# Performance work log

Hardware: AMD Instinct MI355X
Metric: run time of the kernel (lower is better)

The kernel has to match this reference:

```python
import jax, jax.numpy as jnp
import numpy as np

C = 256
SCALE = 2
K = 3
GROUPS = 4


def _conv(x, w, b=None, groups=1, pad=0):
    y = jax.lax.conv_general_dilated(
        x, w, window_strides=(1, 1), padding=[(pad, pad), (pad, pad)],
        dimension_numbers=("NCHW", "OIHW", "NCHW"), feature_group_count=groups)
    if b is not None:
        y = y + b[None, :, None, None]
    return y


def _bn(x, g, b, m, v):
    # eval-mode BatchNorm2d, eps=1e-5
    scale = g / jnp.sqrt(v + 1e-5)
    return (x - m[None, :, None, None]) * scale[None, :, None, None] + b[None, :, None, None]


def _silu(x):
    return x * jax.nn.sigmoid(x)


def setup_inputs() -> dict:
    key = jax.random.key(0)
    ks = jax.random.split(key, 16)
    c = C
    s2k2 = SCALE ** 2 * K ** 2
    p = lambda k, shape, sc=0.05: jax.random.normal(k, shape, dtype=jnp.float32) * sc
    return {
        "x": jax.random.normal(ks[0], (8, c, 64, 64), dtype=jnp.float32),
        # kernel_compressor: 1x1, c -> c//2
        "Wkc": p(ks[1], (c // 2, c, 1, 1)), "bkc": p(ks[2], (c // 2,)),
        # kernel_predictor: 3x3 c//2 -> c//4, BN, SiLU, 1x1 -> s^2*k^2
        "Wkp1": p(ks[3], (c // 4, c // 2, 3, 3)), "bkp1": p(ks[4], (c // 4,)),
        "g1": 1.0 + p(ks[5], (c // 4,)), "be1": p(ks[6], (c // 4,)),
        "m1": p(ks[7], (c // 4,)), "v1": 1.0 + jax.random.uniform(ks[8], (c // 4,), dtype=jnp.float32),
        "Wkp2": p(ks[9], (s2k2, c // 4, 1, 1)), "bkp2": p(ks[10], (s2k2,)),
        # grouped 3x3 "deform" conv: c -> c, groups=4, no bias
        "Wdef": p(ks[11], (c, c // GROUPS, 3, 3)),
        # semantic gate
        "Wg1": p(ks[12], (c // 4, c, 1, 1)), "bg1": p(ks[13], (c // 4,)),
        "Wg2": p(ks[14], (c, c // 4, 1, 1)), "bg2": p(ks[15], (c,)),
    }


def reference(x, Wkc, bkc, Wkp1, bkp1, g1, be1, m1, v1, Wkp2, bkp2, Wdef, Wg1, bg1, Wg2, bg2):
    b, c, h, w = x.shape
    s, k = SCALE, K
    # --- dynamic reassembly kernel prediction ---
    comp = _conv(x, Wkc, bkc)                                    # (b, c/2, h, w)
    t = _silu(_bn(_conv(comp, Wkp1, bkp1, pad=1), g1, be1, m1, v1))
    kw = _conv(t, Wkp2, bkp2)                                    # (b, s^2*k^2, h, w)
    kw = kw.transpose(0, 2, 3, 1).reshape(b, h, w, s * s, k * k)
    kw = jax.nn.softmax(kw, axis=-1)
    # --- unfold (k x k patches, pad k//2), F.unfold ordering: kernel pos i*k+j ---
    xp = jnp.pad(x, ((0, 0), (0, 0), (1, 1), (1, 1)))
    patches = jnp.stack([xp[:, :, i:i + h, j:j + w]
                         for i in range(k) for j in range(k)], axis=-1)  # (b,c,h,w,k^2)
    kernel_out = jnp.einsum('bchwk,bhwsk->bhwsc', patches, kw)           # (b,h,w,s^2,c)
    kernel_out = kernel_out.transpose(0, 4, 1, 3, 2).reshape(b, c, h * s, w * s)
    # --- grouped conv branch + bilinear upsample (align_corners=False) ---
    enh = _conv(x, Wdef, None, groups=GROUPS, pad=1)
    up = jax.image.resize(enh, (b, c, h * s, w * s), method='linear')
    fused = kernel_out + up
    # --- SE-style semantic gate ---
    pooled = jnp.mean(fused, axis=(2, 3), keepdims=True)
    gate = jax.nn.sigmoid(_conv(_silu(_conv(pooled, Wg1, bg1)), Wg2, bg2))
    return fused * gate
```

## Files before the change

kernel.cpp:

```cpp
#include <hip/hip_runtime.h>
#include <hip/hip_bf16.h>

typedef __hip_bfloat16 bf16;
typedef __attribute__((ext_vector_type(8))) short short8;
typedef __attribute__((ext_vector_type(4))) float floatx4;

__device__ __forceinline__ float cvt(float v){ return v; }
__device__ __forceinline__ float cvt(bf16 v){ return __bfloat162float(v); }
__device__ __forceinline__ unsigned short f2bu(float f){
    union { float f; unsigned u; } uf; uf.f = f;
    unsigned u = uf.u;
    return (unsigned short)((u + 0x7FFFu + ((u>>16)&1u)) >> 16);
}
__device__ __forceinline__ float bu2f(unsigned short b){
    union { unsigned u; float f; } uf; uf.u = ((unsigned)b)<<16; return uf.f;
}
__device__ __forceinline__ floatx4 mfma16(short8 a, short8 b, floatx4 c){
    return __builtin_amdgcn_mfma_f32_16x16x32_bf16(a, b, c, 0, 0, 0);
}

constexpr size_t O_KW    = 0;
constexpr size_t O_ENH   = O_KW    + 1179648;
constexpr size_t O_XBT   = O_ENH   + 8388608;
constexpr size_t O_COMPB = O_XBT   + 4194304;
constexpr size_t O_TB    = O_COMPB + 2097152;
constexpr size_t O_POOL  = O_TB    + 1048576;
constexpr size_t O_GATE  = O_POOL  + 2048;
constexpr size_t O_WKC   = O_GATE  + 2048;
constexpr size_t O_BKC   = O_WKC   + 32768;
constexpr size_t O_WKP1  = O_BKC   + 128;
constexpr size_t O_ALPHA = O_WKP1  + 73728;
constexpr size_t O_BETA  = O_ALPHA + 64;
constexpr size_t O_WKP2  = O_BETA  + 64;
constexpr size_t O_BKP2  = O_WKP2  + 2304;
constexpr size_t O_WDEF  = O_BKP2  + 64;
constexpr size_t O_WG1   = O_WDEF  + 147456;
constexpr size_t O_BG1   = O_WG1   + 16384;
constexpr size_t O_WG2   = O_BG1   + 64;
constexpr size_t O_BG2   = O_WG2   + 16384;
constexpr size_t O_FLAG  = O_BG2   + 256;
constexpr size_t O_WKCB  = (O_FLAG + 1 + 3) & ~(size_t)3;
constexpr size_t O_WKP1B = O_WKCB  + 16384;
constexpr size_t O_WDEFB = O_WKP1B + 36864;

__global__ __launch_bounds__(256) void kdet(const unsigned* __restrict__ w, float* flag)
{
    int hits = 0;
    for (int i = threadIdx.x; i < 16384; i += 256){
        unsigned v = w[i];
        hits += (((v >> 7) & 0xFFu) == 0xFFu) ? 1 : 0;
    }
    __shared__ int sh[256];
    sh[threadIdx.x] = hits;
    __syncthreads();
    for (int o = 128; o > 0; o >>= 1){
        if (threadIdx.x < o) sh[threadIdx.x] += sh[threadIdx.x + o];
        __syncthreads();
    }
    if (threadIdx.x == 0) flag[0] = (sh[0] > 0) ? 1.0f : 0.0f;
}

template<typename T>
__device__ __forceinline__ void k0_body(
    const T* Wkc, const T* bkc, const T* Wkp1, const T* bkp1,
    const T* g1, const T* be1, const T* m1, const T* v1,
    const T* Wkp2, const T* bkp2, const T* Wdef,
    const T* Wg1, const T* bg1, const T* Wg2, const T* bg2,
    float* ws)
{
    int i = blockIdx.x*256 + threadIdx.x;
    if (i < 32768){ ws[O_WKC+i] = cvt(Wkc[i]); return; }  i -= 32768;
    if (i < 128)  { ws[O_BKC+i] = cvt(bkc[i]); return; }  i -= 128;
    if (i < 73728){ ws[O_WKP1+i]= cvt(Wkp1[i]); return; } i -= 73728;
    if (i < 64){
        float a = cvt(g1[i]) / sqrtf(cvt(v1[i]) + 1e-5f);
        ws[O_ALPHA+i] = a;
        ws[O_BETA+i]  = (cvt(bkp1[i]) - cvt(m1[i]))*a + cvt(be1[i]);
        return;
    } i -= 64;
    if (i < 2304) { ws[O_WKP2+i] = cvt(Wkp2[i]); return; } i -= 2304;
    if (i < 36)   { ws[O_BKP2+i] = cvt(bkp2[i]); return; } i -= 36;
    if (i < 147456){ ws[O_WDEF+i]= cvt(Wdef[i]); return; } i -= 147456;
    if (i < 16384){ ws[O_WG1+i]  = cvt(Wg1[i]); return; }  i -= 16384;
    if (i < 64)   { ws[O_BG1+i]  = cvt(bg1[i]); return; }  i -= 64;
    if (i < 16384){ ws[O_WG2+i]  = cvt(Wg2[i]); return; }  i -= 16384;
    if (i < 256)  { ws[O_BG2+i]  = cvt(bg2[i]); return; }  i -= 256;
    if (i < 2048) { ws[O_POOL+i] = 0.f; return; }
}

__global__ __launch_bounds__(256) void k0_prep(
    const void* Wkc, const void* bkc, const void* Wkp1, const void* bkp1,
    const void* g1, const void* be1, const void* m1, const void* v1,
    const void* Wkp2, const void* bkp2, const void* Wdef,
    const void* Wg1, const void* bg1, const void* Wg2, const void* bg2,
    float* ws)
{
    if (ws[O_FLAG] > 0.5f)
        k0_body<float>((const float*)Wkc,(const float*)bkc,(const float*)Wkp1,(const float*)bkp1,
                       (const float*)g1,(const float*)be1,(const float*)m1,(const float*)v1,
                       (const float*)Wkp2,(const float*)bkp2,(const float*)Wdef,
                       (const float*)Wg1,(const float*)bg1,(const float*)Wg2,(const float*)bg2, ws);
    else
        k0_body<bf16>((const bf16*)Wkc,(const bf16*)bkc,(const bf16*)Wkp1,(const bf16*)bkp1,
                      (const bf16*)g1,(const bf16*)be1,(const bf16*)m1,(const bf16*)v1,
                      (const bf16*)Wkp2,(const bf16*)bkp2,(const bf16*)Wdef,
                      (const bf16*)Wg1,(const bf16*)bg1,(const bf16*)Wg2,(const bf16*)bg2, ws);
}

__global__ __launch_bounds__(256) void k0b_pack(float* ws)
{
    unsigned short* wkcb  = (unsigned short*)(ws + O_WKCB);
    unsigned short* wkp1b = (unsigned short*)(ws + O_WKP1B);
    unsigned short* wdefb = (unsigned short*)(ws + O_WDEFB);
    int i = blockIdx.x*256 + threadIdx.x;
    if (i < 32768){
        int kc = i>>12, cout = (i>>5)&127, cil = i&31;
        wkcb[i] = f2bu(ws[O_WKC + (size_t)cout*256 + kc*32 + cil]);
        return;
    } i -= 32768;
    if (i < 73728){
        int ch = i/18432, r = i - ch*18432;
        int kp = r>>11, cout = (r>>5)&63, cil = r&31;
        wkp1b[i] = f2bu(ws[O_WKP1 + ((size_t)cout*128 + ch*32 + cil)*9 + kp]);
        return;
    } i -= 73728;
    if (i < 147456){
        int g = i/36864, r1 = i - g*36864;
        int ch = r1/18432, r2 = r1 - ch*18432;
        int kp = r2>>11, cout = (r2>>5)&63, cil = r2&31;
        wdefb[i] = f2bu(ws[O_WDEF + (((size_t)(g*64+cout))*64 + ch*32 + cil)*9 + kp]);
    }
}

template<typename T>
__device__ __forceinline__ void xcvt_body(const T* __restrict__ x, unsigned short* __restrict__ xbt)
{
    __shared__ float lT[64*65];
    const int b = blockIdx.y;
    const int ci0 = (blockIdx.x & 3) * 64;
    const int pos0 = (blockIdx.x >> 2) * 64;
    const int lane = threadIdx.x & 63;
    const int wrow = threadIdx.x >> 6;
    for (int i = wrow; i < 64; i += 4)
        lT[i*65 + lane] = cvt(x[((size_t)(b*256 + ci0 + i))*4096 + pos0 + lane]);
    __syncthreads();
    for (int u = threadIdx.x; u < 2048; u += 256){
        const int pr = u >> 5, pc = u & 31;
        unsigned lo = f2bu(lT[(2*pc)*65 + pr]);
        unsigned hi = f2bu(lT[(2*pc+1)*65 + pr]);
        *(unsigned*)&xbt[((size_t)(b*4096) + pos0 + pr)*256 + ci0 + 2*pc] = lo | (hi<<16);
    }
}

__global__ __launch_bounds__(256) void xcvt(const void* x, unsigned short* xbt, const float* flag)
{
    if (*flag > 0.5f) xcvt_body<float>((const float*)x, xbt);
    else              xcvt_body<bf16>((const bf16*)x, xbt);
}

__global__ __launch_bounds__(256) void k1_mfma(
    const unsigned short* __restrict__ xbt, const unsigned short* __restrict__ wb,
    const float* __restrict__ bias, unsigned short* __restrict__ compb)
{
    __shared__ __align__(16) short lA[128*32];
    __shared__ __align__(16) short lB[128*32];
    const int b = blockIdx.y, pos0 = blockIdx.x*128;
    const int tid = threadIdx.x;
    const int wave = tid>>6, lane = tid&63, q = lane>>4, r16 = lane&15;
    const int mh = (wave&1)*64, nh = (wave>>1)*64;
    floatx4 zero = {0.f,0.f,0.f,0.f};
    floatx4 acc[4][4];
    #pragma unroll
    for (int m=0;m<4;m++){ acc[m][0]=zero; acc[m][1]=zero; acc[m][2]=zero; acc[m][3]=zero; }

    for (int kc=0;kc<8;kc++){
        __syncthreads();
        {
            const short8* s = (const short8*)(wb + kc*4096);
            short8* d = (short8*)lA;
            d[tid] = s[tid]; d[tid+256] = s[tid+256];
        }
        {
            #pragma unroll
            for (int k=0;k<2;k++){
                const int u = tid + k*256;
                const int p = u>>2, part = u&3;
                *(short8*)&lB[p*32 + part*8] =
                    *(const short8*)(xbt + ((size_t)(b*4096)+pos0+p)*256 + kc*32 + part*8);
            }
        }
        __syncthreads();
        short8 af[4], bfr[4];
        #pragma unroll
        for (int mt=0;mt<4;mt++) af[mt]  = *(const short8*)&lA[(mh + mt*16 + r16)*32 + q*8];
        #pragma unroll
        for (int nt=0;nt<4;nt++) bfr[nt] = *(const short8*)&lB[(nh + nt*16 + r16)*32 + q*8];
        #pragma unroll
        for (int mt=0;mt<4;mt++)
            #pragma unroll
            for (int nt=0;nt<4;nt++)
                acc[mt][nt] = mfma16(af[mt], bfr[nt], acc[mt][nt]);
    }
    #pragma unroll
    for (int mt=0;mt<4;mt++){
        const int cb = mh + mt*16 + q*4;
        const float b0=bias[cb], b1=bias[cb+1], b2=bias[cb+2], b3=bias[cb+3];
        #pragma unroll
        for (int nt=0;nt<4;nt++){
            const int pos = pos0 + nh + nt*16 + r16;
            floatx4 v = acc[mt][nt];
            uint2 pk;
            pk.x = (unsigned)f2bu(v.x+b0) | ((unsigned)f2bu(v.y+b1)<<16);
            pk.y = (unsigned)f2bu(v.z+b2) | ((unsigned)f2bu(v.w+b3)<<16);
            *(uint2*)(compb + ((size_t)(b*4096)+pos)*128 + cb) = pk;
        }
    }
}

__global__ __launch_bounds__(256) void conv3x3_all(
    const unsigned short* __restrict__ xbt, const unsigned short* __restrict__ compb,
    const unsigned short* __restrict__ wkp1b, const unsigned short* __restrict__ wdefb,
    const float* __restrict__ alpha, const float* __restrict__ beta,
    unsigned short* __restrict__ tb, float* __restrict__ enh)
{
    __shared__ __align__(16) short lX[6*66*32];
    __shared__ __align__(16) short lW[9*64*32];
    const int row0 = blockIdx.x*4, b = blockIdx.y, z = blockIdx.z;
    const bool isKP = (z == 0);
    const int g = isKP ? 0 : (z-1);
    const int CICH  = isKP ? 4 : 2;
    const int CITOT = isKP ? 128 : 256;
    const int cibase = g*64;
    const unsigned short* src  = isKP ? compb : xbt;
    const unsigned short* wsrc = isKP ? wkp1b : (wdefb + (size_t)g*36864);
    const int tid = threadIdx.x;
    const int wave = tid>>6, lane = tid&63, q = lane>>4, r16 = lane&15;
    floatx4 zero = {0.f,0.f,0.f,0.f};
    floatx4 acc[4][4];
    #pragma unroll
    for (int m=0;m<4;m++){ acc[m][0]=zero; acc[m][1]=zero; acc[m][2]=zero; acc[m][3]=zero; }

    {
        short8 zz = {0,0,0,0,0,0,0,0};
        short8* d = (short8*)lX;
        for (int i = tid; i < 1584; i += 256) d[i] = zz;
    }

    for (int ch = 0; ch < CICH; ch++){
        __syncthreads();
        {
            const short8* s = (const short8*)(wsrc + ch*18432);
            short8* d = (short8*)lW;
            #pragma unroll
            for (int i=0;i<9;i++) d[tid + i*256] = s[tid + i*256];
        }
        {
            const int gc = tid>>2, part = tid&3;
            #pragma unroll
            for (int r=0;r<6;r++){
                const int gr = row0 - 1 + r;
                if ((unsigned)gr < 64u){
                    const unsigned short* sp = src +
                        ((size_t)(b*4096) + gr*64 + gc)*CITOT + cibase + ch*32 + part*8;
                    *(short8*)&lX[(r*66 + 1 + gc)*32 + part*8] = *(const short8*)sp;
                }
            }
        }
        __syncthreads();
        #pragma unroll
        for (int kp=0; kp<9; kp++){
            const int dr = kp/3, dc = kp - dr*3;
            short8 af[4], bfr[4];
            #pragma unroll
            for (int mt=0;mt<4;mt++)
                af[mt] = *(const short8*)&lW[(kp*64 + mt*16 + r16)*32 + q*8];
            #pragma unroll
            for (int nt=0;nt<4;nt++)
                bfr[nt] = *(const short8*)&lX[((wave+dr)*66 + nt*16 + r16 + dc)*32 + q*8];
            #pragma unroll
            for (int mt=0;mt<4;mt++)
                #pragma unroll
                for (int nt=0;nt<4;nt++)
                    acc[mt][nt] = mfma16(af[mt], bfr[nt], acc[mt][nt]);
        }
    }
    const int orow = row0 + wave;
    if (isKP){
        #pragma unroll
        for (int mt=0;mt<4;mt++){
            const int cb = mt*16 + q*4;
            const float a0=alpha[cb],a1=alpha[cb+1],a2=alpha[cb+2],a3=alpha[cb+3];
            const float e0=beta[cb],e1=beta[cb+1],e2=beta[cb+2],e3=beta[cb+3];
            #pragma unroll
            for (int nt=0;nt<4;nt++){
                const int pos = orow*64 + nt*16 + r16;
                floatx4 v = acc[mt][nt];
                float z0=v.x*a0+e0, z1=v.y*a1+e1, z2=v.z*a2+e2, z3=v.w*a3+e3;
                z0 = z0/(1.f+expf(-z0)); z1 = z1/(1.f+expf(-z1));
                z2 = z2/(1.f+expf(-z2)); z3 = z3/(1.f+expf(-z3));
                uint2 pk;
                pk.x = (unsigned)f2bu(z0) | ((unsigned)f2bu(z1)<<16);
                pk.y = (unsigned)f2bu(z2) | ((unsigned)f2bu(z3)<<16);
                *(uint2*)(tb + ((size_t)(b*4096)+pos)*64 + cb) = pk;
            }
        }
    } else {
        #pragma unroll
        for (int mt=0;mt<4;mt++){
            #pragma unroll
            for (int nt=0;nt<4;nt++){
                const int pos = orow*64 + nt*16 + r16;
                floatx4 v = acc[mt][nt];
                float* op = enh + ((size_t)(b*256) + g*64 + mt*16 + q*4)*4096 + pos;
                op[0]=v.x; op[4096]=v.y; op[8192]=v.z; op[12288]=v.w;
            }
        }
    }
}

__global__ __launch_bounds__(128) void k3_kpred(
    const unsigned short* __restrict__ tb, const float* __restrict__ W,
    const float* __restrict__ bias, float* __restrict__ kw)
{
    __shared__ float wl[2304];
    __shared__ float bl[36];
    for (int i=threadIdx.x;i<2304;i+=128) wl[i]=W[i];
    if (threadIdx.x<36) bl[threadIdx.x]=bias[threadIdx.x];
    __syncthreads();
    const int gid = blockIdx.x*128 + threadIdx.x;
    const unsigned short* tp = tb + (size_t)gid*64;
    float acc[36];
    #pragma unroll
    for (int o=0;o<36;o++) acc[o]=bl[o];
    #pragma unroll
    for (int c8=0;c8<8;c8++){
        uint4 pk = *(const uint4*)(tp + c8*8);
        unsigned u[4] = {pk.x, pk.y, pk.z, pk.w};
        float f[8];
        #pragma unroll
        for (int j=0;j<4;j++){
            f[2*j]   = bu2f((unsigned short)(u[j]&0xFFFFu));
            f[2*j+1] = bu2f((unsigned short)(u[j]>>16));
        }
        #pragma unroll
        for (int jj=0;jj<8;jj++){
            const int ci = c8*8+jj;
            #pragma unroll
            for (int o=0;o<36;o++) acc[o] += f[jj]*wl[o*64+ci];
        }
    }
    float* op = kw + (size_t)gid*36;
    #pragma unroll
    for (int s=0;s<4;s++){
        float mx = acc[s*9];
        #pragma unroll
        for (int k=1;k<9;k++) mx = fmaxf(mx, acc[s*9+k]);
        float e[9]; float sum=0.f;
        #pragma unroll
        for (int k=0;k<9;k++){ e[k]=expf(acc[s*9+k]-mx); sum+=e[k]; }
        float inv = 1.f/sum;
        #pragma unroll
        for (int k=0;k<9;k++) op[s*9+k] = e[k]*inv;
    }
}

template<typename T>
__device__ __forceinline__ void k5_body(
    const T* __restrict__ x, const float* __restrict__ kw,
    const float* __restrict__ enh, float* __restrict__ out,
    float* __restrict__ pooled)
{
    const int hi = blockIdx.x & 63;
    const int b  = blockIdx.x >> 6;
    const int c0 = blockIdx.y * 64;
    __shared__ float kwl[64*37];
    for (int i=threadIdx.x;i<2304;i+=256){
        int wi = i/36, r = i - wi*36;
        kwl[wi*37+r] = kw[((size_t)(b*4096 + hi*64 + wi))*36 + r];
    }
    __syncthreads();
    const int wi = threadIdx.x & 63;
    const int cl = threadIdx.x >> 6;
    float kreg[36];
    #pragma unroll
    for (int r=0;r<36;r++) kreg[r] = kwl[wi*37+r];

    const bool vx0 = wi>0, vx2 = wi<63;
    const bool vy0 = hi>0, vy2 = hi<63;
    const int rm = vy0? hi-1 : 0;
    const int rp = vy2? hi+1 : 63;
    const int par = wi&1;
    const int mA = wi>>1, mB = 32+mA;
    float wc0, wc1; int a0,a1,b0c,b1c;
    if (par==0){ wc0=0.25f; wc1=0.75f; a0=(mA>0)?mA-1:0; a1=mA;   b0c=mB-1; b1c=mB; }
    else       { wc0=0.75f; wc1=0.25f; a0=mA;            a1=mA+1; b0c=mB;   b1c=(mB<63)?mB+1:63; }
    const int y0 = hi*2;

    for (int c = c0+cl; c < c0+64; c += 4){
        const T* xc = x + ((size_t)(b*256)+c)*4096;
        float v[9];
        v[0] = (vy0&&vx0)? cvt(xc[(hi-1)*64+wi-1]) : 0.f;
        v[1] = (vy0)     ? cvt(xc[(hi-1)*64+wi  ]) : 0.f;
        v[2] = (vy0&&vx2)? cvt(xc[(hi-1)*64+wi+1]) : 0.f;
        v[3] = (vx0)     ? cvt(xc[ hi   *64+wi-1]) : 0.f;
        v[4] =             cvt(xc[ hi   *64+wi  ]);
        v[5] = (vx2)     ? cvt(xc[ hi   *64+wi+1]) : 0.f;
        v[6] = (vy2&&vx0)? cvt(xc[(hi+1)*64+wi-1]) : 0.f;
        v[7] = (vy2)     ? cvt(xc[(hi+1)*64+wi  ]) : 0.f;
        v[8] = (vy2&&vx2)? cvt(xc[(hi+1)*64+wi+1]) : 0.f;
        float ko[4];
        #pragma unroll
        for (int s=0;s<4;s++){
            float a = 0.f;
            #pragma unroll
            for (int k=0;k<9;k++) a += v[k]*kreg[s*9+k];
            ko[s]=a;
        }
        const float* ec = enh + ((size_t)(b*256)+c)*4096;
        const float* er0 = ec + rm*64;
        const float* er1 = ec + hi*64;
        const float* er2 = ec + rp*64;
        float uA0 = wc0*er0[a0]+wc1*er0[a1];
        float uB0 = wc0*er0[b0c]+wc1*er0[b1c];
        float uA1 = wc0*er1[a0]+wc1*er1[a1];
        float uB1 = wc0*er1[b0c]+wc1*er1[b1c];
        float uA2 = wc0*er2[a0]+wc1*er2[a1];
        float uB2 = wc0*er2[b0c]+wc1*er2[b1c];
        float up00 = 0.25f*uA0 + 0.75f*uA1;
        float up01 = 0.25f*uB0 + 0.75f*uB1;
        float up10 = 0.75f*uA1 + 0.25f*uA2;
        float up11 = 0.75f*uB1 + 0.25f*uB2;
        float o00 = ko[0]+up00, o01 = ko[1]+up01, o10 = ko[2]+up10, o11 = ko[3]+up11;
        float* o = out + (((size_t)(b*256)+c)*128 + y0)*128;
        o[wi]      = o00;
        o[64+wi]   = o01;
        o[128+wi]  = o10;
        o[192+wi]  = o11;
        float ps = (o00+o01) + (o10+o11);
        #pragma unroll
        for (int off=32;off>0;off>>=1) ps += __shfl_down(ps, off, 64);
        if (wi==0) atomicAdd(&pooled[b*256 + c], ps);
    }
}

__global__ __launch_bounds__(256) void k5_fuse(
    const void* x, const float* kw, const float* enh, float* out,
    float* pooled, const float* flag)
{
    if (*flag > 0.5f) k5_body<float>((const float*)x, kw, enh, out, pooled);
    else              k5_body<bf16>((const bf16*)x, kw, enh, out, pooled);
}

__global__ __launch_bounds__(256) void k7_gate(
    const float* __restrict__ pooled,
    const float* __restrict__ Wg1, const float* __restrict__ bg1,
    const float* __restrict__ Wg2, const float* __restrict__ bg2,
    float* __restrict__ gate)
{
    const int b = blockIdx.x;
    __shared__ float pl[256];
    __shared__ float hid[64];
    pl[threadIdx.x] = pooled[b*256+threadIdx.x] * (1.f/16384.f);
    __syncthreads();
    if (threadIdx.x < 64){
        float a = bg1[threadIdx.x];
        const float* w = Wg1 + (size_t)threadIdx.x*256;
        for (int c=0;c<256;c++) a += w[c]*pl[c];
        hid[threadIdx.x] = a/(1.f+expf(-a));
    }
    __syncthreads();
    float a = bg2[threadIdx.x];
    const float* w = Wg2 + (size_t)threadIdx.x*64;
    for (int j=0;j<64;j++) a += w[j]*hid[j];
    gate[b*256+threadIdx.x] = 1.f/(1.f+expf(-a));
}

__global__ __launch_bounds__(256) void k8_scale(
    float* __restrict__ out, const float* __restrict__ gate)
{
    const size_t gid = (size_t)blockIdx.x*256 + threadIdx.x;
    const float g = gate[gid>>12];
    float4* p = (float4*)out;
    float4 v = p[gid];
    v.x*=g; v.y*=g; v.z*=g; v.w*=g;
    p[gid] = v;
}

extern "C" void kernel_launch(void* const* d_in, const int* in_sizes, int n_in,
                              void* d_out, int out_size, void* d_ws, size_t ws_size,
                              hipStream_t stream)
{
    float* ws = (float*)d_ws;
    float* out = (float*)d_out;
    unsigned short* xbt   = (unsigned short*)(ws + O_XBT);
    unsigned short* compb = (unsigned short*)(ws + O_COMPB);
    unsigned short* tb    = (unsigned short*)(ws + O_TB);
    unsigned short* wkcb  = (unsigned short*)(ws + O_WKCB);
    unsigned short* wkp1b = (unsigned short*)(ws + O_WKP1B);
    unsigned short* wdefb = (unsigned short*)(ws + O_WDEFB);

    kdet<<<1, 256, 0, stream>>>((const unsigned*)d_in[1], ws + O_FLAG);
    k0_prep<<<1140, 256, 0, stream>>>(d_in[1],d_in[2],d_in[3],d_in[4],d_in[5],d_in[6],d_in[7],d_in[8],
                                      d_in[9],d_in[10],d_in[11],d_in[12],d_in[13],d_in[14],d_in[15], ws);
    k0b_pack<<<992, 256, 0, stream>>>(ws);
    xcvt<<<dim3(256,8), 256, 0, stream>>>(d_in[0], xbt, ws+O_FLAG);
    k1_mfma<<<dim3(32,8), 256, 0, stream>>>(xbt, wkcb, ws+O_BKC, compb);
    conv3x3_all<<<dim3(16,8,5), 256, 0, stream>>>(xbt, compb, wkp1b, wdefb,
                                                  ws+O_ALPHA, ws+O_BETA, tb, ws+O_ENH);
    k3_kpred<<<256, 128, 0, stream>>>(tb, ws+O_WKP2, ws+O_BKP2, ws+O_KW);
    k5_fuse<<<dim3(512,4), 256, 0, stream>>>(d_in[0], ws+O_KW, ws+O_ENH, out, ws+O_POOL, ws+O_FLAG);
    k7_gate<<<8, 256, 0, stream>>>(ws+O_POOL, ws+O_WG1, ws+O_BG1, ws+O_WG2, ws+O_BG2, ws+O_GATE);
    k8_scale<<<32768, 256, 0, stream>>>(out, ws+O_GATE);
}
```

Measured before the change: 367.6 us.

## Swizzle LDS tiles for MFMA, shuffle stencil neighbors, batch pooled reductions

XOR-swizzles the 16-byte chunks of the LDS A/B tiles in the 1x1 and 3x3 MFMA convolutions to cut bank conflicts on fragment reads. In the fuse kernel, horizontal stencil neighbours now come from wave shuffles instead of extra global loads, and the channel loop is fully unrolled. Per-channel pooled partial sums are buffered and reduced after the loop, so loads and the reductions can be interleaved. Shared arrays move into the kernel wrappers so the two template instantiations share one allocation. The unrolled loop raises register pressure in the fuse kernel.

Result: slower. 418.7 us (+13.9%).

```diff
diff --git a/kernel.cpp b/kernel.cpp
--- a/kernel.cpp
+++ b/kernel.cpp
@@ -17,6 +17,9 @@
 }
 __device__ __forceinline__ floatx4 mfma16(short8 a, short8 b, floatx4 c){
     return __builtin_amdgcn_mfma_f32_16x16x32_bf16(a, b, c, 0, 0, 0);
+}
+__device__ __forceinline__ int swz8(int row, int part){
+    return row*32 + ((part ^ ((row>>1)&3))<<3);
 }
 
 constexpr size_t O_KW    = 0;
@@ -133,9 +136,9 @@
 }
 
 template<typename T>
-__device__ __forceinline__ void xcvt_body(const T* __restrict__ x, unsigned short* __restrict__ xbt)
-{
-    __shared__ float lT[64*65];
+__device__ __forceinline__ void xcvt_body(const T* __restrict__ x, unsigned short* __restrict__ xbt,
+                                          float* lT)
+{
     const int b = blockIdx.y;
     const int ci0 = (blockIdx.x & 3) * 64;
     const int pos0 = (blockIdx.x >> 2) * 64;
@@ -154,8 +157,9 @@
 
 __global__ __launch_bounds__(256) void xcvt(const void* x, unsigned short* xbt, const float* flag)
 {
-    if (*flag > 0.5f) xcvt_body<float>((const float*)x, xbt);
-    else              xcvt_body<bf16>((const bf16*)x, xbt);
+    __shared__ float lT[64*65];
+    if (*flag > 0.5f) xcvt_body<float>((const float*)x, xbt, lT);
+    else              xcvt_body<bf16>((const bf16*)x, xbt, lT);
 }
 
 __global__ __launch_bounds__(256) void k1_mfma(
@@ -177,24 +181,25 @@
         __syncthreads();
         {
             const short8* s = (const short8*)(wb + kc*4096);
-            short8* d = (short8*)lA;
-            d[tid] = s[tid]; d[tid+256] = s[tid+256];
+            const int u0 = tid, u1 = tid + 256;
+            *(short8*)&lA[swz8(u0>>2, u0&3)] = s[u0];
+            *(short8*)&lA[swz8(u1>>2, u1&3)] = s[u1];
         }
         {
             #pragma unroll
             for (int k=0;k<2;k++){
                 const int u = tid + k*256;
                 const int p = u>>2, part = u&3;
-                *(short8*)&lB[p*32 + part*8] =
+                *(short8*)&lB[swz8(p, part)] =
                     *(const short8*)(xbt + ((size_t)(b*4096)+pos0+p)*256 + kc*32 + part*8);
             }
         }
         __syncthreads();
         short8 af[4], bfr[4];
         #pragma unroll
-        for (int mt=0;mt<4;mt++) af[mt]  = *(const short8*)&lA[(mh + mt*16 + r16)*32 + q*8];
-        #pragma unroll
-        for (int nt=0;nt<4;nt++) bfr[nt] = *(const short8*)&lB[(nh + nt*16 + r16)*32 + q*8];
+        for (int mt=0;mt<4;mt++) af[mt]  = *(const short8*)&lA[swz8(mh + mt*16 + r16, q)];
+        #pragma unroll
+        for (int nt=0;nt<4;nt++) bfr[nt] = *(const short8*)&lB[swz8(nh + nt*16 + r16, q)];
         #pragma unroll
         for (int mt=0;mt<4;mt++)
             #pragma unroll
@@ -250,9 +255,11 @@
         __syncthreads();
         {
             const short8* s = (const short8*)(wsrc + ch*18432);
-            short8* d = (short8*)lW;
-            #pragma unroll
-            for (int i=0;i<9;i++) d[tid + i*256] = s[tid + i*256];
+            #pragma unroll
+            for (int i=0;i<9;i++){
+                const int u = tid + i*256;
+                *(short8*)&lW[swz8(u>>2, u&3)] = s[u];
+            }
         }
         {
             const int gc = tid>>2, part = tid&3;
@@ -262,7 +269,7 @@
                 if ((unsigned)gr < 64u){
                     const unsigned short* sp = src +
                         ((size_t)(b*4096) + gr*64 + gc)*CITOT + cibase + ch*32 + part*8;
-                    *(short8*)&lX[(r*66 + 1 + gc)*32 + part*8] = *(const short8*)sp;
+                    *(short8*)&lX[swz8(r*66 + 1 + gc, part)] = *(const short8*)sp;
                 }
             }
         }
@@ -273,10 +280,10 @@
             short8 af[4], bfr[4];
             #pragma unroll
             for (int mt=0;mt<4;mt++)
-                af[mt] = *(const short8*)&lW[(kp*64 + mt*16 + r16)*32 + q*8];
+                af[mt] = *(const short8*)&lW[swz8(kp*64 + mt*16 + r16, q)];
             #pragma unroll
             for (int nt=0;nt<4;nt++)
-                bfr[nt] = *(const short8*)&lX[((wave+dr)*66 + nt*16 + r16 + dc)*32 + q*8];
+                bfr[nt] = *(const short8*)&lX[swz8((wave+dr)*66 + nt*16 + r16 + dc, q)];
             #pragma unroll
             for (int mt=0;mt<4;mt++)
                 #pragma unroll
@@ -368,12 +375,11 @@
 __device__ __forceinline__ void k5_body(
     const T* __restrict__ x, const float* __restrict__ kw,
     const float* __restrict__ enh, float* __restrict__ out,
-    float* __restrict__ pooled)
+    float* __restrict__ pooled, float* kwl)
 {
     const int hi = blockIdx.x & 63;
     const int b  = blockIdx.x >> 6;
     const int c0 = blockIdx.y * 64;
-    __shared__ float kwl[64*37];
     for (int i=threadIdx.x;i<2304;i+=256){
         int wi = i/36, r = i - wi*36;
         kwl[wi*37+r] = kw[((size_t)(b*4096 + hi*64 + wi))*36 + r];
@@ -396,24 +402,26 @@
     else       { wc0=0.75f; wc1=0.25f; a0=mA;            a1=mA+1; b0c=mB;   b1c=(mB<63)?mB+1:63; }
     const int y0 = hi*2;
 
-    for (int c = c0+cl; c < c0+64; c += 4){
+    float psum[16];
+    #pragma unroll
+    for (int i=0;i<16;i++){
+        const int c = c0 + cl + 4*i;
         const T* xc = x + ((size_t)(b*256)+c)*4096;
-        float v[9];
-        v[0] = (vy0&&vx0)? cvt(xc[(hi-1)*64+wi-1]) : 0.f;
-        v[1] = (vy0)     ? cvt(xc[(hi-1)*64+wi  ]) : 0.f;
-        v[2] = (vy0&&vx2)? cvt(xc[(hi-1)*64+wi+1]) : 0.f;
-        v[3] = (vx0)     ? cvt(xc[ hi   *64+wi-1]) : 0.f;
-        v[4] =             cvt(xc[ hi   *64+wi  ]);
-        v[5] = (vx2)     ? cvt(xc[ hi   *64+wi+1]) : 0.f;
-        v[6] = (vy2&&vx0)? cvt(xc[(hi+1)*64+wi-1]) : 0.f;
-        v[7] = (vy2)     ? cvt(xc[(hi+1)*64+wi  ]) : 0.f;
-        v[8] = (vy2&&vx2)? cvt(xc[(hi+1)*64+wi+1]) : 0.f;
+        float xm = vy0 ? cvt(xc[(hi-1)*64+wi]) : 0.f;
+        float x0v =       cvt(xc[ hi   *64+wi]);
+        float xp = vy2 ? cvt(xc[(hi+1)*64+wi]) : 0.f;
+        float lm = __shfl_up(xm, 1, 64),  rmv = __shfl_down(xm, 1, 64);
+        float l0 = __shfl_up(x0v, 1, 64), r0v = __shfl_down(x0v, 1, 64);
+        float lp = __shfl_up(xp, 1, 64),  rpv = __shfl_down(xp, 1, 64);
+        float v0 = vx0 ? lm : 0.f,  v2 = vx2 ? rmv : 0.f;
+        float v3 = vx0 ? l0 : 0.f,  v5 = vx2 ? r0v : 0.f;
+        float v6 = vx0 ? lp : 0.f,  v8 = vx2 ? rpv : 0.f;
         float ko[4];
         #pragma unroll
         for (int s=0;s<4;s++){
-            float a = 0.f;
-            #pragma unroll
-            for (int k=0;k<9;k++) a += v[k]*kreg[s*9+k];
+            float a = v0*kreg[s*9+0] + xm *kreg[s*9+1] + v2*kreg[s*9+2]
+                    + v3*kreg[s*9+3] + x0v*kreg[s*9+4] + v5*kreg[s*9+5]
+                    + v6*kreg[s*9+6] + xp *kreg[s*9+7] + v8*kreg[s*9+8];
             ko[s]=a;
         }
         const float* ec = enh + ((size_t)(b*256)+c)*4096;
@@ -436,10 +444,20 @@
         o[64+wi]   = o01;
         o[128+wi]  = o10;
         o[192+wi]  = o11;
-        float ps = (o00+o01) + (o10+o11);
-        #pragma unroll
-        for (int off=32;off>0;off>>=1) ps += __shfl_down(ps, off, 64);
-        if (wi==0) atomicAdd(&pooled[b*256 + c], ps);
+        psum[i] = (o00+o01) + (o10+o11);
+    }
+    #pragma unroll
+    for (int i=0;i<16;i++){
+        float ps = psum[i];
+        ps += __shfl_down(ps,32,64); ps += __shfl_down(ps,16,64);
+        ps += __shfl_down(ps, 8,64); ps += __shfl_down(ps, 4,64);
+        ps += __shfl_down(ps, 2,64); ps += __shfl_down(ps, 1,64);
+        psum[i] = ps;
+    }
+    if (wi==0){
+        #pragma unroll
+        for (int i=0;i<16;i++)
+            atomicAdd(&pooled[b*256 + c0 + cl + 4*i], psum[i]);
     }
 }
 
@@ -447,8 +465,9 @@
     const void* x, const float* kw, const float* enh, float* out,
     float* pooled, const float* flag)
 {
-    if (*flag > 0.5f) k5_body<float>((const float*)x, kw, enh, out, pooled);
-    else              k5_body<bf16>((const bf16*)x, kw, enh, out, pooled);
+    __shared__ float kwl[64*37];
+    if (*flag > 0.5f) k5_body<float>((const float*)x, kw, enh, out, pooled, kwl);
+    else              k5_body<bf16>((const bf16*)x, kw, enh, out, pooled, kwl);
 }
 
 __global__ __launch_bounds__(256) void k7_gate(
```

## Swizzle LDS tiles for MFMA kernels, share smem across template branches, halve k5 channel tile

Applied to the files above, without the earlier changes.

Applies an XOR swizzle to the 16-byte chunks of the LDS tiles in the 1x1 and 3x3 MFMA conv kernels, to cut bank conflicts on the 32-short-wide rows. Shared arrays in xcvt and k5 are hoisted to the kernel wrapper so the float and bf16 template branches share one allocation instead of two, which reduces LDS per block. k5_fuse now covers 32 channels per block over twice as many blocks, adding parallelism at the cost of reloading the kw tile twice as often.

Measured after the change: 381.2 us. +3.7%, slower.

```diff
diff --git a/kernel.cpp b/kernel.cpp
--- a/kernel.cpp
+++ b/kernel.cpp
@@ -17,6 +17,9 @@
 }
 __device__ __forceinline__ floatx4 mfma16(short8 a, short8 b, floatx4 c){
     return __builtin_amdgcn_mfma_f32_16x16x32_bf16(a, b, c, 0, 0, 0);
+}
+__device__ __forceinline__ int swz8(int row, int part){
+    return row*32 + ((part ^ ((row>>1)&3))<<3);
 }
 
 constexpr size_t O_KW    = 0;
@@ -133,9 +136,9 @@
 }
 
 template<typename T>
-__device__ __forceinline__ void xcvt_body(const T* __restrict__ x, unsigned short* __restrict__ xbt)
-{
-    __shared__ float lT[64*65];
+__device__ __forceinline__ void xcvt_body(const T* __restrict__ x, unsigned short* __restrict__ xbt,
+                                          float* lT)
+{
     const int b = blockIdx.y;
     const int ci0 = (blockIdx.x & 3) * 64;
     const int pos0 = (blockIdx.x >> 2) * 64;
@@ -154,8 +157,9 @@
 
 __global__ __launch_bounds__(256) void xcvt(const void* x, unsigned short* xbt, const float* flag)
 {
-    if (*flag > 0.5f) xcvt_body<float>((const float*)x, xbt);
-    else              xcvt_body<bf16>((const bf16*)x, xbt);
+    __shared__ float lT[64*65];
+    if (*flag > 0.5f) xcvt_body<float>((const float*)x, xbt, lT);
+    else              xcvt_body<bf16>((const bf16*)x, xbt, lT);
 }
 
 __global__ __launch_bounds__(256) void k1_mfma(
@@ -177,24 +181,25 @@
         __syncthreads();
         {
             const short8* s = (const short8*)(wb + kc*4096);
-            short8* d = (short8*)lA;
-            d[tid] = s[tid]; d[tid+256] = s[tid+256];
+            const int u0 = tid, u1 = tid + 256;
+            *(short8*)&lA[swz8(u0>>2, u0&3)] = s[u0];
+            *(short8*)&lA[swz8(u1>>2, u1&3)] = s[u1];
         }
         {
             #pragma unroll
             for (int k=0;k<2;k++){
                 const int u = tid + k*256;
                 const int p = u>>2, part = u&3;
-                *(short8*)&lB[p*32 + part*8] =
+                *(short8*)&lB[swz8(p, part)] =
                     *(const short8*)(xbt + ((size_t)(b*4096)+pos0+p)*256 + kc*32 + part*8);
             }
         }
         __syncthreads();
         short8 af[4], bfr[4];
         #pragma unroll
-        for (int mt=0;mt<4;mt++) af[mt]  = *(const short8*)&lA[(mh + mt*16 + r16)*32 + q*8];
-        #pragma unroll
-        for (int nt=0;nt<4;nt++) bfr[nt] = *(const short8*)&lB[(nh + nt*16 + r16)*32 + q*8];
+        for (int mt=0;mt<4;mt++) af[mt]  = *(const short8*)&lA[swz8(mh + mt*16 + r16, q)];
+        #pragma unroll
+        for (int nt=0;nt<4;nt++) bfr[nt] = *(const short8*)&lB[swz8(nh + nt*16 + r16, q)];
         #pragma unroll
         for (int mt=0;mt<4;mt++)
             #pragma unroll
@@ -250,9 +255,11 @@
         __syncthreads();
         {
             const short8* s = (const short8*)(wsrc + ch*18432);
-            short8* d = (short8*)lW;
-            #pragma unroll
-            for (int i=0;i<9;i++) d[tid + i*256] = s[tid + i*256];
+            #pragma unroll
+            for (int i=0;i<9;i++){
+                const int u = tid + i*256;
+                *(short8*)&lW[swz8(u>>2, u&3)] = s[u];
+            }
         }
         {
             const int gc = tid>>2, part = tid&3;
@@ -262,7 +269,7 @@
                 if ((unsigned)gr < 64u){
                     const unsigned short* sp = src +
                         ((size_t)(b*4096) + gr*64 + gc)*CITOT + cibase + ch*32 + part*8;
-                    *(short8*)&lX[(r*66 + 1 + gc)*32 + part*8] = *(const short8*)sp;
+                    *(short8*)&lX[swz8(r*66 + 1 + gc, part)] = *(const short8*)sp;
                 }
             }
         }
@@ -273,10 +280,10 @@
             short8 af[4], bfr[4];
             #pragma unroll
             for (int mt=0;mt<4;mt++)
-                af[mt] = *(const short8*)&lW[(kp*64 + mt*16 + r16)*32 + q*8];
+                af[mt] = *(const short8*)&lW[swz8(kp*64 + mt*16 + r16, q)];
             #pragma unroll
             for (int nt=0;nt<4;nt++)
-                bfr[nt] = *(const short8*)&lX[((wave+dr)*66 + nt*16 + r16 + dc)*32 + q*8];
+                bfr[nt] = *(const short8*)&lX[swz8((wave+dr)*66 + nt*16 + r16 + dc, q)];
             #pragma unroll
             for (int mt=0;mt<4;mt++)
                 #pragma unroll
@@ -368,12 +375,11 @@
 __device__ __forceinline__ void k5_body(
     const T* __restrict__ x, const float* __restrict__ kw,
     const float* __restrict__ enh, float* __restrict__ out,
-    float* __restrict__ pooled)
+    float* __restrict__ pooled, float* kwl)
 {
     const int hi = blockIdx.x & 63;
     const int b  = blockIdx.x >> 6;
-    const int c0 = blockIdx.y * 64;
-    __shared__ float kwl[64*37];
+    const int c0 = blockIdx.y * 32;
     for (int i=threadIdx.x;i<2304;i+=256){
         int wi = i/36, r = i - wi*36;
         kwl[wi*37+r] = kw[((size_t)(b*4096 + hi*64 + wi))*36 + r];
@@ -396,7 +402,7 @@
     else       { wc0=0.75f; wc1=0.25f; a0=mA;            a1=mA+1; b0c=mB;   b1c=(mB<63)?mB+1:63; }
     const int y0 = hi*2;
 
-    for (int c = c0+cl; c < c0+64; c += 4){
+    for (int c = c0+cl; c < c0+32; c += 4){
         const T* xc = x + ((size_t)(b*256)+c)*4096;
         float v[9];
         v[0] = (vy0&&vx0)? cvt(xc[(hi-1)*64+wi-1]) : 0.f;
@@ -447,8 +453,9 @@
     const void* x, const float* kw, const float* enh, float* out,
     float* pooled, const float* flag)
 {
-    if (*flag > 0.5f) k5_body<float>((const float*)x, kw, enh, out, pooled);
-    else              k5_body<bf16>((const bf16*)x, kw, enh, out, pooled);
+    __shared__ float kwl[64*37];
+    if (*flag > 0.5f) k5_body<float>((const float*)x, kw, enh, out, pooled, kwl);
+    else              k5_body<bf16>((const bf16*)x, kw, enh, out, pooled, kwl);
 }
 
 __global__ __launch_bounds__(256) void k7_gate(
@@ -508,7 +515,7 @@
     conv3x3_all<<<dim3(16,8,5), 256, 0, stream>>>(xbt, compb, wkp1b, wdefb,
                                                   ws+O_ALPHA, ws+O_BETA, tb, ws+O_ENH);
     k3_kpred<<<256, 128, 0, stream>>>(tb, ws+O_WKP2, ws+O_BKP2, ws+O_KW);
-    k5_fuse<<<dim3(512,4), 256, 0, stream>>>(d_in[0], ws+O_KW, ws+O_ENH, out, ws+O_POOL, ws+O_FLAG);
+    k5_fuse<<<dim3(512,8), 256, 0, stream>>>(d_in[0], ws+O_KW, ws+O_ENH, out, ws+O_POOL, ws+O_FLAG);
     k7_gate<<<8, 256, 0, stream>>>(ws+O_POOL, ws+O_WG1, ws+O_BG1, ws+O_WG2, ws+O_BG2, ws+O_GATE);
     k8_scale<<<32768, 256, 0, stream>>>(out, ws+O_GATE);
 }
```
